# Kernel optimization log

Hardware: AMD Instinct MI355X
Metric: run time of the kernel (lower is better)

The kernel has to match this reference:

```python
import jax, jax.numpy as jnp
import numpy as np

D = 4096
L = 24
H = 8
HD = D // H
Z_TAU = 3.0
SCALE = 1.0 / float(np.sqrt(HD))


def _ln(x, w=None, b=None, eps=1e-5):
    # torch F.layer_norm over last dim; affine optional
    m = jnp.mean(x, axis=-1, keepdims=True)
    v = jnp.var(x, axis=-1, keepdims=True)
    y = (x - m) * jax.lax.rsqrt(v + eps)
    if w is not None:
        y = y * w + b
    return y


def setup_inputs() -> dict:
    key = jax.random.key(0)
    ks = jax.random.split(key, 16)
    T, N = 512, 2048
    s = 0.02  # init scale for weights
    inp = {
        'text_features': jax.random.normal(ks[0], (T, D), jnp.float32),
        'layer_features': jax.random.normal(ks[1], (L, N, D), jnp.float32),
        # DynamicSharingUnit params
        'layer_embed': jax.random.normal(ks[2], (L, D), jnp.float32) * s,
        'Wc_w': jax.random.normal(ks[3], (2 * D, D), jnp.float32) * s,
        'Wc_b': jnp.zeros((D,), jnp.float32),
        'Wz_w': jax.random.normal(ks[4], (4 * D, D), jnp.float32) * s,
        'Wz_b': jnp.full((D,), -2.0, jnp.float32),
        # SpatialGate params (delta MLP + alpha)
        'd1_w': jax.random.normal(ks[5], (D, D), jnp.float32) * s,
        'd1_b': jnp.zeros((D,), jnp.float32),
        'd2_w': jax.random.normal(ks[6], (D, D), jnp.float32) * s,
        'd2_b': jnp.zeros((D,), jnp.float32),
        'alpha': jnp.asarray(0.5, jnp.float32),
        # attention projections
        'Wq_w': jax.random.normal(ks[7], (D, D), jnp.float32) * s,
        'Wq_b': jnp.zeros((D,), jnp.float32),
        'Wk_w': jax.random.normal(ks[8], (D, D), jnp.float32) * s,
        'Wk_b': jnp.zeros((D,), jnp.float32),
        'Wo_w': jax.random.normal(ks[9], (D, D), jnp.float32) * s,
        'Wo_b': jnp.zeros((D,), jnp.float32),
        # layernorm affine params
        'qn_w': jnp.ones((D,), jnp.float32), 'qn_b': jnp.zeros((D,), jnp.float32),
        'kn_w': jnp.ones((D,), jnp.float32), 'kn_b': jnp.zeros((D,), jnp.float32),
        'vn_w': jnp.ones((D,), jnp.float32), 'vn_b': jnp.zeros((D,), jnp.float32),
        'on_w': jnp.ones((D,), jnp.float32), 'on_b': jnp.zeros((D,), jnp.float32),
    }
    return inp


def reference(text_features, layer_features, layer_embed, Wc_w, Wc_b, Wz_w, Wz_b,
              d1_w, d1_b, d2_w, d2_b, alpha,
              Wq_w, Wq_b, Wk_w, Wk_b, Wo_w, Wo_b,
              qn_w, qn_b, kn_w, kn_b, vn_w, vn_b, on_w, on_b):
    T = text_features.shape[0]
    dt = text_features.dtype

    text_global = _ln(jnp.mean(text_features, axis=0))  # [D]
    y = jnp.mean(layer_features, axis=1)                # [L, D] per-layer means

    # sequential 24-step DynamicSharingUnit recurrence
    def step(c_prev, xs):
        y_l, e_l = xs
        c_tilde = jnp.tanh(jnp.concatenate([y_l, e_l], axis=-1) @ Wc_w + Wc_b)
        z_logit = jnp.concatenate([y_l, c_prev, e_l, text_global], axis=-1) @ Wz_w + Wz_b
        z = jax.nn.sigmoid(z_logit / Z_TAU)
        c_l = c_prev + z * (c_tilde - c_prev)
        return c_l, c_l

    c0 = jnp.zeros((D,), dt)
    _, contexts = jax.lax.scan(step, c0, (y, layer_embed))  # [L, D]

    c_23 = contexts[-2]            # context after layer index 22
    pre_23 = layer_features[-2]    # [N, D]

    # SpatialGate: x + tanh(alpha) * tanh(MLP(LN(x + c)))
    h = _ln(pre_23 + c_23[None, :])
    delta = jnp.tanh(jax.nn.gelu(h @ d1_w + d1_b, approximate=False) @ d2_w + d2_b)
    refreshed = pre_23 + jnp.tanh(alpha) * delta  # [N, D]

    Q = _ln(text_features @ Wq_w + Wq_b, qn_w, qn_b)  # [T, D]
    K = _ln(refreshed @ Wk_w + Wk_b, kn_w, kn_b)      # [N, D]
    V = _ln(refreshed, vn_w, vn_b)                    # [N, D]

    q = Q.reshape(T, H, HD)
    k = K.reshape(-1, H, HD)
    v = V.reshape(-1, H, HD)
    scores = jnp.einsum('thd,nhd->htn', q, k) * SCALE  # [H, T, N]
    w = jax.nn.softmax(scores, axis=-1)
    attn = jnp.einsum('htn,nhd->thd', w, v).reshape(T, D)

    return _ln(attn @ Wo_w + Wo_b, on_w, on_b)  # [T, D]
```

## Files before the change

kernel.cpp:

```cpp
#include <hip/hip_runtime.h>
#include <hip/hip_bf16.h>

constexpr int D_  = 4096;
constexpr int L_  = 24;
constexpr int T_  = 512;
constexpr int N_  = 2048;
constexpr int H_  = 8;
constexpr int HD_ = 512;
constexpr float SCALE_ = 0.04419417382415922f;

typedef __attribute__((ext_vector_type(8))) short short8;
typedef __attribute__((ext_vector_type(4))) float f32x4;

__device__ __forceinline__ unsigned short f2b(float f){
  union{float f; unsigned u;} v; v.f=f;
  return (unsigned short)((v.u + 0x7fffu + ((v.u>>16)&1u))>>16);
}
__device__ __forceinline__ float b2f(unsigned short h){
  union{unsigned u; float f;} v; v.u=((unsigned)h)<<16; return v.f;
}

__device__ __forceinline__ void gload_lds16(const unsigned short* g, unsigned short* l){
  __builtin_amdgcn_global_load_lds((const __attribute__((address_space(1))) unsigned int*)g,
                                   (__attribute__((address_space(3))) unsigned int*)l, 16, 0, 0);
}

struct TP5 { const float* in[5]; unsigned short* out[5]; };

__global__ void prepass_all(TP5 a, const float* __restrict__ wzc_f,
                            unsigned short* __restrict__ wzcb,
                            const float* __restrict__ text,
                            unsigned short* __restrict__ txb){
  const int z = blockIdx.z, t = threadIdx.x;
  if(z < 5){
    __shared__ float tile[64][65];
    const float* in = a.in[z];
    unsigned short* out = a.out[z];
    const int k0 = blockIdx.x*64, n0 = blockIdx.y*64;
    const int tr = t>>6, tc = t&63;
#pragma unroll
    for(int i=0;i<16;++i) tile[i*4+tr][tc] = in[(size_t)(k0+i*4+tr)*D_ + n0+tc];
    __syncthreads();
#pragma unroll
    for(int i=0;i<16;++i) out[(size_t)(n0+i*4+tr)*D_ + k0+tc] = f2b(tile[tc][i*4+tr]);
  } else {
    const int bb = blockIdx.y*64 + blockIdx.x;
    const float* in; unsigned short* out; size_t base;
    if(z < 7){ in = wzc_f; out = wzcb; base = ((size_t)(z-5)*4096 + bb)*2048 + (size_t)t*8; }
    else { if(bb >= 1024) return; in = text; out = txb; base = (size_t)bb*2048 + (size_t)t*8; }
    const float4 x0 = *(const float4*)(in + base);
    const float4 x1 = *(const float4*)(in + base + 4);
    unsigned short o[8] __attribute__((aligned(16)));
    o[0]=f2b(x0.x);o[1]=f2b(x0.y);o[2]=f2b(x0.z);o[3]=f2b(x0.w);
    o[4]=f2b(x1.x);o[5]=f2b(x1.y);o[6]=f2b(x1.z);o[7]=f2b(x1.w);
    *(uint4*)(out + base) = *(const uint4*)o;
  }
}

__global__ void transpose_head_b(const unsigned short* __restrict__ in,
                                 unsigned short* __restrict__ out){
  __shared__ unsigned short tile[64][65];
  const int t = threadIdx.x;
  const int h = blockIdx.z;
  const int d0 = blockIdx.x*64, n0 = blockIdx.y*64;
  const int tr = t>>6, tc = t&63;
#pragma unroll
  for(int i=0;i<16;++i) tile[i*4+tr][tc] = in[(size_t)(n0+i*4+tr)*D_ + h*HD_ + d0+tc];
  __syncthreads();
#pragma unroll
  for(int i=0;i<16;++i) out[((size_t)h*HD_ + d0+i*4+tr)*N_ + n0+tc] = tile[tc][i*4+tr];
}

__global__ void colsum_all(const float* __restrict__ layers, const float* __restrict__ text,
                           float* __restrict__ part){
  const int d = blockIdx.x*256 + threadIdx.x;
  const int s = blockIdx.y, z = blockIdx.z;
  const float* p; int rows;
  if(z < 23){ p = layers + (size_t)z*N_*D_ + (size_t)s*(N_/8)*D_ + d; rows = N_/8; }
  else      { p = text + (size_t)s*(T_/8)*D_ + d; rows = T_/8; }
  float acc = 0.f;
  for(int r=0;r<rows;++r) acc += p[(size_t)r*D_];
  part[((size_t)z*8 + s)*D_ + d] = acc;
}

__global__ void reduce_y_gm(const float* __restrict__ part, float* __restrict__ y,
                            float* __restrict__ tg){
  __shared__ float sm[256];
  const int b = blockIdx.x, t = threadIdx.x;
  if(b < 368){
    const int i = b*256 + t, l = i>>12, j = i & (D_-1);
    float a = 0.f;
#pragma unroll
    for(int s=0;s<8;++s) a += part[((size_t)l*8 + s)*D_ + j];
    y[i] = a * (1.f/N_);
    return;
  }
  float v[16]; float sum = 0.f;
#pragma unroll
  for(int c=0;c<16;++c){
    const int j = c*256 + t;
    float a = 0.f;
#pragma unroll
    for(int s=0;s<8;++s) a += part[((size_t)184 + s)*D_ + j];
    v[c] = a * (1.f/T_); sum += v[c];
  }
  sm[t]=sum; __syncthreads();
  for(int o=128;o>0;o>>=1){ if(t<o) sm[t]+=sm[t+o]; __syncthreads(); }
  const float mean = sm[0]*(1.f/D_); __syncthreads();
  float q=0.f;
#pragma unroll
  for(int c=0;c<16;++c){ const float dd=v[c]-mean; q+=dd*dd; }
  sm[t]=q; __syncthreads();
  for(int o=128;o>0;o>>=1){ if(t<o) sm[t]+=sm[t+o]; __syncthreads(); }
  const float rstd = rsqrtf(sm[0]*(1.f/D_) + 1e-5f);
#pragma unroll
  for(int c=0;c<16;++c) tg[c*256+t] = (v[c]-mean)*rstd;
}

__global__ void smallm_all(const float* __restrict__ Wc, const float* __restrict__ Wz,
                           const float* __restrict__ y, const float* __restrict__ e,
                           const float* __restrict__ tg,
                           float* __restrict__ part0, float* __restrict__ part1){
  const int j = blockIdx.x*256 + threadIdx.x;
  const int sIdx = blockIdx.y;
  const bool w1 = (sIdx >= 16);
  const int s = w1 ? sIdx-16 : sIdx;
  const float* W = w1 ? Wz : Wc;
  const int k0 = s * 512;
  float acc[L_];
#pragma unroll
  for(int l=0;l<L_;++l) acc[l]=0.f;
  __shared__ float xs[L_][64];
  for(int kc=0; kc<512; kc+=64){
    __syncthreads();
    for(int i=threadIdx.x; i<L_*64; i+=256){
      const int l=i>>6, kk=i&63, k=k0+kc+kk;
      float xv;
      if(!w1) xv = (k<D_)? y[(size_t)l*D_+k] : e[(size_t)l*D_ + (k-D_)];
      else    xv = (k<D_)? y[(size_t)l*D_+k]
                : ((k<2*D_)? e[(size_t)l*D_ + (k-D_)] : tg[k-2*D_]);
      xs[l][kk]=xv;
    }
    __syncthreads();
    for(int kk=0;kk<64;++kk){
      const int k=k0+kc+kk;
      const int wrow = w1 ? ((k<D_)? k : k+D_) : k;
      const float wv = W[(size_t)wrow*D_ + j];
#pragma unroll
      for(int l=0;l<L_;++l) acc[l] += xs[l][kk]*wv;
    }
  }
  float* out = w1 ? part1 : part0;
  const int S = w1 ? 24 : 16;
  for(int l=0;l<L_;++l) out[((size_t)l*S + s)*D_ + j] = acc[l];
}

__global__ void reduce_ct_aall(const float* __restrict__ part0, const float* __restrict__ part1,
                               const float* __restrict__ Wcb, const float* __restrict__ Wzb,
                               float* __restrict__ ct, float* __restrict__ aall){
  int b = blockIdx.x;
  const int t = threadIdx.x;
  if(b < 368){
    const int i = b*256+t, l = i>>12, j = i & (D_-1);
    float a = 0.f;
#pragma unroll
    for(int s=0;s<16;++s) a += part0[((size_t)l*16 + s)*D_ + j];
    ct[i] = tanhf(a + Wcb[j]);
  } else {
    b -= 368;
    const int i = b*256+t, l = i>>12, j = i & (D_-1);
    float a = 0.f;
#pragma unroll
    for(int s=0;s<24;++s) a += part1[((size_t)l*24 + s)*D_ + j];
    aall[i] = a + Wzb[j];
  }
}

__device__ __forceinline__ void rec_matvec(const unsigned short* __restrict__ Wzc,
                                           const float* cs, float* red, float* __restrict__ zcur,
                                           int cg, int ks, int t){
  const int k0 = ks*128;
  float acc[8];
#pragma unroll
  for(int q=0;q<8;++q) acc[q]=0.f;
  const int rg = t>>6, oc = t&63;
  const unsigned short* Wb = Wzc + (size_t)(k0+rg*32)*D_ + cg*512 + oc*8;
#pragma unroll
  for(int rr=0;rr<4;++rr){
#pragma unroll
    for(int r=0;r<8;++r){
      const uint4 wv = *(const uint4*)(Wb + (size_t)(rr*8+r)*D_);
      const float cv = cs[rg*32+rr*8+r];
      acc[0]+=cv*b2f((unsigned short)(wv.x&0xffffu));
      acc[1]+=cv*b2f((unsigned short)(wv.x>>16));
      acc[2]+=cv*b2f((unsigned short)(wv.y&0xffffu));
      acc[3]+=cv*b2f((unsigned short)(wv.y>>16));
      acc[4]+=cv*b2f((unsigned short)(wv.z&0xffffu));
      acc[5]+=cv*b2f((unsigned short)(wv.z>>16));
      acc[6]+=cv*b2f((unsigned short)(wv.w&0xffffu));
      acc[7]+=cv*b2f((unsigned short)(wv.w>>16));
    }
  }
#pragma unroll
  for(int q=0;q<8;++q) red[rg*512 + oc*8 + q] = acc[q];
  __syncthreads();
  float s0=0.f, s1=0.f;
#pragma unroll
  for(int g=0;g<4;++g){ s0 += red[g*512 + t]; s1 += red[g*512 + t + 256]; }
  zcur[(size_t)ks*D_ + cg*512 + t]       = s0;
  zcur[(size_t)ks*D_ + cg*512 + t + 256] = s1;
}

__global__ __launch_bounds__(256,2) void rec_first(
    const unsigned short* __restrict__ Wzc, const float* __restrict__ aall0,
    const float* __restrict__ ct0, float* __restrict__ zcur, float* __restrict__ cnew){
  const int blk = blockIdx.x, cg = blk & 7, ks = blk >> 3, t = threadIdx.x;
  const int k0 = ks*128;
  __shared__ float cs[128];
  __shared__ float red[4*512];
  if(t<128){
    const float zl = aall0[k0+t];
    const float z = 1.f/(1.f+expf(-zl*(1.f/3.f)));
    const float cn = z*ct0[k0+t];
    cs[t]=cn; if(cg==0) cnew[k0+t]=cn;
  }
  __syncthreads();
  rec_matvec(Wzc, cs, red, zcur, cg, ks, t);
}

__global__ __launch_bounds__(256,2) void rec_step(
    const unsigned short* __restrict__ Wzc,
    const float* __restrict__ zprev, float* __restrict__ zcur,
    const float* __restrict__ cprev, float* __restrict__ cnew,
    const float* __restrict__ aallL, const float* __restrict__ ctL){
  const int blk = blockIdx.x, cg = blk & 7, ks = blk >> 3, t = threadIdx.x;
  const int k0 = ks*128;
  __shared__ float cs[128];
  __shared__ float red[4*512];
  {
    const int col = t & 127, hf = t >> 7;
    float s=0.f;
#pragma unroll
    for(int si=0;si<16;++si) s += zprev[(size_t)(hf*16+si)*D_ + k0 + col];
    red[hf*128+col] = s;
    __syncthreads();
    if(t<128){
      const float zl = aallL[k0+t] + red[t] + red[128+t];
      const float z = 1.f/(1.f+expf(-zl*(1.f/3.f)));
      const float cp = cprev[k0+t];
      const float cn = cp + z*(ctL[k0+t]-cp);
      cs[t]=cn;
      if(cg==0) cnew[k0+t]=cn;
    }
  }
  __syncthreads();
  rec_matvec(Wzc, cs, red, zcur, cg, ks, t);
}

__global__ void gate_final(const float* __restrict__ zp, const float* __restrict__ cin,
                           const float* __restrict__ aallL, const float* __restrict__ ctL,
                           float* __restrict__ cout){
  const int j = blockIdx.x*256 + threadIdx.x;
  float zl = aallL[j];
  for(int s=0;s<32;++s) zl += zp[(size_t)s*D_ + j];
  const float z = 1.f/(1.f + expf(-zl*(1.f/3.f)));
  const float cp = cin[j];
  cout[j] = cp + z*(ctL[j] - cp);
}

__device__ __forceinline__ void ln_body(const float* xr, const float* cvec,
                                        const float* w, const float* b,
                                        float* of, unsigned short* ob,
                                        bool addc, bool aff, bool obf, float* sm, int t){
  float v[16]; float s=0.f;
#pragma unroll
  for(int i=0;i<16;++i){
    const int d = i*256 + t;
    float val = xr[d];
    if(addc) val += cvec[d];
    v[i]=val; s+=val;
  }
  sm[t]=s; __syncthreads();
  for(int o=128;o>0;o>>=1){ if(t<o) sm[t]+=sm[t+o]; __syncthreads(); }
  const float mean = sm[0]*(1.f/D_); __syncthreads();
  float q=0.f;
#pragma unroll
  for(int i=0;i<16;++i){ const float dd=v[i]-mean; q+=dd*dd; }
  sm[t]=q; __syncthreads();
  for(int o=128;o>0;o>>=1){ if(t<o) sm[t]+=sm[t+o]; __syncthreads(); }
  const float rstd = rsqrtf(sm[0]*(1.f/D_) + 1e-5f);
#pragma unroll
  for(int i=0;i<16;++i){
    const int d = i*256+t;
    float yv=(v[i]-mean)*rstd;
    if(aff) yv = yv*w[d] + b[d];
    if(obf) ob[d] = f2b(yv);
    else    of[d] = yv;
  }
}

template<bool ADDC, bool AFF, bool OBF>
__global__ void row_ln(const float* __restrict__ x, const float* __restrict__ cvec,
                       const float* __restrict__ w, const float* __restrict__ b,
                       float* __restrict__ of, unsigned short* __restrict__ ob){
  __shared__ float sm[256];
  const int row = blockIdx.x, t = threadIdx.x;
  ln_body(x + (size_t)row*D_, cvec, w, b,
          of? of + (size_t)row*D_ : nullptr, ob? ob + (size_t)row*D_ : nullptr,
          ADDC, AFF, OBF, sm, t);
}

__global__ void ln3(const float* __restrict__ qpre, const float* __restrict__ refr,
                    const float* __restrict__ kpre,
                    const float* __restrict__ qnw, const float* __restrict__ qnb,
                    const float* __restrict__ vnw, const float* __restrict__ vnb,
                    const float* __restrict__ knw, const float* __restrict__ knb,
                    unsigned short* __restrict__ qb, unsigned short* __restrict__ vb,
                    unsigned short* __restrict__ kb){
  __shared__ float sm[256];
  const int which = blockIdx.y, row = blockIdx.x, t = threadIdx.x;
  const float *x, *w, *b; unsigned short* o;
  if(which==0){ if(row>=T_) return; x=qpre; w=qnw; b=qnb; o=qb; }
  else if(which==1){ x=refr; w=vnw; b=vnb; o=vb; }
  else { x=kpre; w=knw; b=knb; o=kb; }
  ln_body(x + (size_t)row*D_, nullptr, w, b, nullptr, o + (size_t)row*D_,
          false, true, true, sm, t);
}

__global__ void softmax_rows(unsigned short* __restrict__ wb){
  __shared__ float sm[256];
  const size_t base = (size_t)blockIdx.x * N_;
  const int t = threadIdx.x;
  float v[8];
  float mx = -3.4e38f;
#pragma unroll
  for(int i=0;i<8;++i){ v[i]=b2f(wb[base + i*256 + t]); mx=fmaxf(mx,v[i]); }
  sm[t]=mx; __syncthreads();
  for(int o=128;o>0;o>>=1){ if(t<o) sm[t]=fmaxf(sm[t],sm[t+o]); __syncthreads(); }
  mx=sm[0]; __syncthreads();
  float s=0.f;
#pragma unroll
  for(int i=0;i<8;++i){ v[i]=expf(v[i]-mx); s+=v[i]; }
  sm[t]=s; __syncthreads();
  for(int o=128;o>0;o>>=1){ if(t<o) sm[t]+=sm[t+o]; __syncthreads(); }
  const float inv = 1.f/sm[0];
#pragma unroll
  for(int i=0;i<8;++i) wb[base + i*256 + t] = f2b(v[i]*inv);
}

enum { EPI_F32_BIAS=0, EPI_BF16_GELU=1, EPI_SPATIAL=2, EPI_BF16_SCALE=3, EPI_BF16=4 };

constexpr int GBK=32;

template<int EPI, int WM>
__global__ __launch_bounds__(256,2) void gemm_bt(
  const unsigned short* __restrict__ A, const unsigned short* __restrict__ BT,
  const float* __restrict__ bias,
  float* __restrict__ Cf, unsigned short* __restrict__ Cb,
  int M, int Ncols, int K, int lda, int ldb, int ldc,
  long long aZ, long long bZ, long long cZ,
  const float* __restrict__ pre, const float* __restrict__ alphap, float scale)
{
  constexpr int BMt = WM*64;
  constexpr int NF  = WM*2;
  __shared__ unsigned short As[BMt*GBK];
  __shared__ unsigned short Bs[128*GBK];
  const int t = threadIdx.x;
  const int lane = t&63, wid = t>>6;
  const int m0 = blockIdx.x*BMt, n0 = blockIdx.y*128;
  A  += (size_t)blockIdx.z*aZ;
  BT += (size_t)blockIdx.z*bZ;
  const size_t coff = (size_t)blockIdx.z*cZ;

  const int srow = wid*16 + (lane>>2);
  const int scol = (lane&3)*8;
  const unsigned short* ag = A  + (size_t)(m0+srow)*lda + scol;
  const unsigned short* bg = BT + (size_t)(n0+srow)*ldb + scol;
  unsigned short* asl = &As[wid*512];
  unsigned short* bsl = &Bs[wid*512];

  f32x4 acc[4][NF];
#pragma unroll
  for(int i=0;i<4;++i)
#pragma unroll
    for(int j=0;j<NF;++j) acc[i][j]=(f32x4){0.f,0.f,0.f,0.f};

  const int wm = (WM==2)? (wid>>1)*64 : 0;
  const int wn = (WM==2)? (wid&1)*64 : wid*32;
  const int lrow=lane&15, lk=(lane>>4)*8;

  for(int k0=0;k0<K;k0+=GBK){
    __syncthreads();
    gload_lds16(ag + k0, asl);
    if(WM==2) gload_lds16(ag + k0 + (size_t)64*lda, asl + 2048);
    gload_lds16(bg + k0, bsl);
    gload_lds16(bg + k0 + (size_t)64*ldb, bsl + 2048);
    __syncthreads();
    short8 af[4], bfr[NF];
#pragma unroll
    for(int i=0;i<4;++i)  af[i]  = *(const short8*)&As[(wm+i*16+lrow)*GBK + lk];
#pragma unroll
    for(int j=0;j<NF;++j) bfr[j] = *(const short8*)&Bs[(wn+j*16+lrow)*GBK + lk];
#pragma unroll
    for(int i=0;i<4;++i)
#pragma unroll
      for(int j=0;j<NF;++j)
        acc[i][j] = __builtin_amdgcn_mfma_f32_16x16x32_bf16(af[i], bfr[j], acc[i][j], 0,0,0);
  }

  float ta=0.f;
  if(EPI==EPI_SPATIAL) ta = tanhf(alphap[0]);
#pragma unroll
  for(int i=0;i<4;++i)
#pragma unroll
    for(int j=0;j<NF;++j){
      const int col = n0 + wn + j*16 + lrow;
      const int rb  = m0 + wm + i*16 + (lane>>4)*4;
#pragma unroll
      for(int r=0;r<4;++r){
        const int row = rb + r;
        const float v = acc[i][j][r];
        const size_t idx = coff + (size_t)row*ldc + col;
        if(EPI==EPI_F32_BIAS){ Cf[idx] = v + bias[col]; }
        else if(EPI==EPI_BF16_GELU){
          const float x=v+bias[col];
          Cb[idx]=f2b(0.5f*x*(1.f+erff(x*0.70710678118f)));
        }
        else if(EPI==EPI_SPATIAL){
          const float x=tanhf(v+bias[col]);
          const float o= pre[(size_t)row*ldc+col] + ta*x;
          Cf[idx]=o; Cb[idx]=f2b(o);
        }
        else if(EPI==EPI_BF16_SCALE){ Cb[idx]=f2b(v*scale); }
        else { Cb[idx]=f2b(v); }
      }
    }
}

constexpr int P_SLOT_A = 128*64;
constexpr int P_SLOT_B = 256*64;
constexpr int P_SLOT_E = P_SLOT_A + P_SLOT_B;

#define MF16(a,b,c) __builtin_amdgcn_mfma_f32_16x16x32_bf16(a,b,c,0,0,0)

template<int EPI, bool SWZ>
__global__ __launch_bounds__(512,2) void gemm8p(
    const unsigned short* __restrict__ A, const unsigned short* __restrict__ BT,
    const float* __restrict__ bias,
    float* __restrict__ Cf, unsigned short* __restrict__ Cb,
    int K, int lda, int ldb, int ldc,
    long long aZ, long long bZ, long long cZ,
    const float* __restrict__ pre, const float* __restrict__ alphap, float scale)
{
  __shared__ unsigned short lds[3*P_SLOT_E];
  const int tid = threadIdx.x;
  const int lane = tid & 63, wid = tid >> 6;
  int mi, ni, zi;
  if(SWZ){
    const int b = blockIdx.x;
    const int swz = (b & 7)*32 + (b >> 3);
    mi = swz >> 4; ni = swz & 15; zi = 0;
  } else { mi = blockIdx.x; ni = blockIdx.y; zi = blockIdx.z; }
  const int m0 = mi*128, n0 = ni*256;
  A  += (size_t)zi*aZ;
  BT += (size_t)zi*bZ;
  const size_t coff = (size_t)zi*cZ;

  const int wm = (wid >> 2)*64, wn = (wid & 3)*64;
  const int lr = lane & 15, lhi = lane >> 4;

  auto stage = [&](int slot, int kt){
    const int k0 = kt*64;
    unsigned short* sA = lds + slot*P_SLOT_E;
    unsigned short* sB = sA + P_SLOT_A;
#pragma unroll
    for(int q=0;q<2;++q){
      const int o = q*8192 + tid*16;
      const int r = o >> 7;
      const int cb = (o & 127) ^ ((r & 7) << 4);
      gload_lds16(A + (size_t)(m0+r)*lda + k0 + (cb>>1), sA + q*4096 + wid*512);
    }
#pragma unroll
    for(int q=0;q<4;++q){
      const int o = q*8192 + tid*16;
      const int r = o >> 7;
      const int cb = (o & 127) ^ ((r & 7) << 4);
      gload_lds16(BT + (size_t)(n0+r)*ldb + k0 + (cb>>1), sB + q*4096 + wid*512);
    }
  };

  auto ldA = [&](const unsigned short* sA, int i, int ks)->short8{
    const int ra = wm + i*16 + lr;
    const int cb = (ks*64 + lhi*16) ^ ((ra & 7) << 4);
    return *(const short8*)((const char*)sA + ra*128 + cb);
  };
  auto ldB = [&](const unsigned short* sB, int j, int ks)->short8{
    const int rb = wn + j*16 + lr;
    const int cb = (ks*64 + lhi*16) ^ ((rb & 7) << 4);
    return *(const short8*)((const char*)sB + rb*128 + cb);
  };

  f32x4 acc[4][4];
#pragma unroll
  for(int i=0;i<4;++i)
#pragma unroll
    for(int j=0;j<4;++j) acc[i][j]=(f32x4){0.f,0.f,0.f,0.f};

  auto tile_compute = [&](const unsigned short* sA, const unsigned short* sB){
#pragma unroll
    for(int ks=0; ks<2; ++ks){
      short8 a0=ldA(sA,0,ks), a1=ldA(sA,1,ks), a2=ldA(sA,2,ks), a3=ldA(sA,3,ks);
      short8 b0=ldB(sB,0,ks), b1=ldB(sB,1,ks);
      __builtin_amdgcn_s_setprio(1);
      acc[0][0]=MF16(a0,b0,acc[0][0]); acc[1][0]=MF16(a1,b0,acc[1][0]);
      acc[2][0]=MF16(a2,b0,acc[2][0]); acc[3][0]=MF16(a3,b0,acc[3][0]);
      acc[0][1]=MF16(a0,b1,acc[0][1]); acc[1][1]=MF16(a1,b1,acc[1][1]);
      acc[2][1]=MF16(a2,b1,acc[2][1]); acc[3][1]=MF16(a3,b1,acc[3][1]);
      __builtin_amdgcn_s_setprio(0);
      __builtin_amdgcn_s_barrier();
      short8 b2=ldB(sB,2,ks), b3=ldB(sB,3,ks);
      __builtin_amdgcn_s_setprio(1);
      acc[0][2]=MF16(a0,b2,acc[0][2]); acc[1][2]=MF16(a1,b2,acc[1][2]);
      acc[2][2]=MF16(a2,b2,acc[2][2]); acc[3][2]=MF16(a3,b2,acc[3][2]);
      acc[0][3]=MF16(a0,b3,acc[0][3]); acc[1][3]=MF16(a1,b3,acc[1][3]);
      acc[2][3]=MF16(a2,b3,acc[2][3]); acc[3][3]=MF16(a3,b3,acc[3][3]);
      __builtin_amdgcn_s_setprio(0);
      if(ks==0) __builtin_amdgcn_s_barrier();
    }
  };

  const int nt = K >> 6;
  stage(0, 0);
  stage(1, 1);
  int cur = 0;
  for(int t=0; t<nt-1; ++t){
    asm volatile("s_waitcnt vmcnt(6)" ::: "memory");
    __builtin_amdgcn_s_barrier();
    int s2 = cur+2; if(s2>=3) s2-=3;
    if(t+2 < nt) stage(s2, t+2);
    const unsigned short* sA = lds + cur*P_SLOT_E;
    tile_compute(sA, sA + P_SLOT_A);
    ++cur; if(cur==3) cur=0;
  }
  asm volatile("s_waitcnt vmcnt(0)" ::: "memory");
  __builtin_amdgcn_s_barrier();
  {
    const unsigned short* sA = lds + cur*P_SLOT_E;
    tile_compute(sA, sA + P_SLOT_A);
  }

  float ta=0.f;
  if(EPI==EPI_SPATIAL) ta = tanhf(alphap[0]);
#pragma unroll
  for(int i=0;i<4;++i)
#pragma unroll
    for(int j=0;j<4;++j){
      const int col = n0 + wn + j*16 + lr;
      const int rb  = m0 + wm + i*16 + lhi*4;
#pragma unroll
      for(int r=0;r<4;++r){
        const int row = rb + r;
        const float v = acc[i][j][r];
        const size_t idx = coff + (size_t)row*ldc + col;
        if(EPI==EPI_F32_BIAS){ Cf[idx] = v + bias[col]; }
        else if(EPI==EPI_BF16_GELU){
          const float x = v + bias[col];
          Cb[idx] = f2b(0.5f*x*(1.f+erff(x*0.70710678118f)));
        }
        else if(EPI==EPI_SPATIAL){
          const float x = tanhf(v + bias[col]);
          const float o = pre[idx] + ta*x;
          Cf[idx]=o; Cb[idx]=f2b(o);
        }
        else if(EPI==EPI_BF16_SCALE){ Cb[idx]=f2b(v*scale); }
      }
    }
}

constexpr size_t OFF_TG   = 0;
constexpr size_t OFF_C    = OFF_TG + (size_t)D_*4;
constexpr size_t OFF_Y    = OFF_C  + (size_t)D_*4;
constexpr size_t OFF_CT   = OFF_Y  + (size_t)L_*D_*4;
constexpr size_t OFF_AA   = OFF_CT + (size_t)L_*D_*4;
constexpr size_t OFF_ZP0  = OFF_AA + (size_t)L_*D_*4;
constexpr size_t OFF_ZP1  = OFF_ZP0 + (size_t)32*D_*4;
constexpr size_t OFF_PART = OFF_ZP1 + (size_t)32*D_*4;
constexpr size_t OFF_QPRE = OFF_PART + (size_t)24*L_*D_*4;
constexpr size_t OFF_REFR = OFF_QPRE + (size_t)T_*D_*4;
constexpr size_t OFF_HB   = OFF_REFR + (size_t)N_*D_*4;
constexpr size_t OFF_G1   = OFF_HB + (size_t)N_*D_*2;
constexpr size_t OFF_KPRE = OFF_HB;
constexpr size_t OFF_QB   = OFF_G1 + (size_t)N_*D_*2;
constexpr size_t OFF_KB   = OFF_QB + (size_t)T_*D_*2;
constexpr size_t OFF_VB   = OFF_KB + (size_t)N_*D_*2;
constexpr size_t OFF_VT   = OFF_VB + (size_t)N_*D_*2;
constexpr size_t OFF_WB   = OFF_VT + (size_t)H_*HD_*N_*2;
constexpr size_t OFF_ATTN = OFF_WB + (size_t)H_*T_*N_*2;
constexpr size_t OFF_W1T  = OFF_ATTN + (size_t)T_*D_*2;
constexpr size_t OFF_W2T  = OFF_W1T + (size_t)D_*D_*2;
constexpr size_t OFF_WKT  = OFF_W2T + (size_t)D_*D_*2;
constexpr size_t OFF_WQT  = OFF_WKT + (size_t)D_*D_*2;
constexpr size_t OFF_WOT  = OFF_WQT + (size_t)D_*D_*2;
constexpr size_t OFF_WZCB = OFF_WOT + (size_t)D_*D_*2;
constexpr size_t OFF_TXB  = OFF_WZCB + (size_t)D_*D_*2;
constexpr size_t OFF_REFB = OFF_TXB + (size_t)T_*D_*2;
constexpr size_t OFF_CA   = OFF_REFB + (size_t)N_*D_*2;
constexpr size_t OFF_CB   = OFF_CA + (size_t)D_*4;

extern "C" void kernel_launch(void* const* d_in, const int* in_sizes, int n_in,
                              void* d_out, int out_size, void* d_ws, size_t ws_size,
                              hipStream_t stream){
  (void)in_sizes; (void)n_in; (void)out_size; (void)ws_size;
  const float* text  = (const float*)d_in[0];
  const float* layers= (const float*)d_in[1];
  const float* le    = (const float*)d_in[2];
  const float* Wc    = (const float*)d_in[3];
  const float* Wcb   = (const float*)d_in[4];
  const float* Wz    = (const float*)d_in[5];
  const float* Wzb   = (const float*)d_in[6];
  const float* d1w   = (const float*)d_in[7];
  const float* d1b   = (const float*)d_in[8];
  const float* d2w   = (const float*)d_in[9];
  const float* d2b   = (const float*)d_in[10];
  const float* alpha = (const float*)d_in[11];
  const float* Wqw=(const float*)d_in[12]; const float* Wqb=(const float*)d_in[13];
  const float* Wkw=(const float*)d_in[14]; const float* Wkb=(const float*)d_in[15];
  const float* Wow=(const float*)d_in[16]; const float* Wob=(const float*)d_in[17];
  const float* qnw=(const float*)d_in[18]; const float* qnb=(const float*)d_in[19];
  const float* knw=(const float*)d_in[20]; const float* knb=(const float*)d_in[21];
  const float* vnw=(const float*)d_in[22]; const float* vnb=(const float*)d_in[23];
  const float* onw=(const float*)d_in[24]; const float* onb=(const float*)d_in[25];
  float* out = (float*)d_out;

  char* w = (char*)d_ws;
  float* tg    = (float*)(w + OFF_TG);
  float* cvec  = (float*)(w + OFF_C);
  float* y     = (float*)(w + OFF_Y);
  float* ct    = (float*)(w + OFF_CT);
  float* aall  = (float*)(w + OFF_AA);
  float* zp0   = (float*)(w + OFF_ZP0);
  float* zp1   = (float*)(w + OFF_ZP1);
  float* part  = (float*)(w + OFF_PART);
  float* part1 = part + (size_t)384*D_;
  float* qpre  = (float*)(w + OFF_QPRE);
  float* opre  = qpre;
  float* refr  = (float*)(w + OFF_REFR);
  float* kpre  = (float*)(w + OFF_KPRE);
  float* cA    = (float*)(w + OFF_CA);
  float* cB    = (float*)(w + OFF_CB);
  unsigned short* hb    = (unsigned short*)(w + OFF_HB);
  unsigned short* g1    = (unsigned short*)(w + OFF_G1);
  unsigned short* qb    = (unsigned short*)(w + OFF_QB);
  unsigned short* kb    = (unsigned short*)(w + OFF_KB);
  unsigned short* vb    = (unsigned short*)(w + OFF_VB);
  unsigned short* vt    = (unsigned short*)(w + OFF_VT);
  unsigned short* wb    = (unsigned short*)(w + OFF_WB);
  unsigned short* attnb = (unsigned short*)(w + OFF_ATTN);
  unsigned short* d1t   = (unsigned short*)(w + OFF_W1T);
  unsigned short* d2t   = (unsigned short*)(w + OFF_W2T);
  unsigned short* wkt   = (unsigned short*)(w + OFF_WKT);
  unsigned short* wqt   = (unsigned short*)(w + OFF_WQT);
  unsigned short* wot   = (unsigned short*)(w + OFF_WOT);
  unsigned short* wzcb  = (unsigned short*)(w + OFF_WZCB);
  unsigned short* txb   = (unsigned short*)(w + OFF_TXB);
  unsigned short* refb  = (unsigned short*)(w + OFF_REFB);

  const dim3 b256(256);
  const float* pre23 = layers + (size_t)(L_-2)*N_*D_;

  TP5 tp; tp.in[0]=d1w; tp.in[1]=d2w; tp.in[2]=Wkw; tp.in[3]=Wqw; tp.in[4]=Wow;
  tp.out[0]=d1t; tp.out[1]=d2t; tp.out[2]=wkt; tp.out[3]=wqt; tp.out[4]=wot;
  prepass_all<<<dim3(64,64,8),b256,0,stream>>>(tp, Wz + (size_t)D_*D_, wzcb, text, txb);

  colsum_all<<<dim3(16,8,24),b256,0,stream>>>(layers, text, part);
  reduce_y_gm<<<dim3(369),b256,0,stream>>>(part, y, tg);
  smallm_all<<<dim3(16,40),b256,0,stream>>>(Wc, Wz, y, le, tg, part, part1);
  reduce_ct_aall<<<dim3(736),b256,0,stream>>>(part, part1, Wcb, Wzb, ct, aall);

  rec_first<<<dim3(256),b256,0,stream>>>(wzcb, aall, ct, zp0, cA);
  for(int i=1;i<L_-2;++i){
    float* zprev = (i&1)? zp0 : zp1;
    float* zcur  = (i&1)? zp1 : zp0;
    float* cprev = (i&1)? cA  : cB;
    float* cnew  = (i&1)? cB  : cA;
    rec_step<<<dim3(256),b256,0,stream>>>(wzcb, zprev, zcur, cprev, cnew,
        aall + (size_t)i*D_, ct + (size_t)i*D_);
  }
  gate_final<<<dim3(16),b256,0,stream>>>(zp1, cB,
      aall + (size_t)(L_-2)*D_, ct + (size_t)(L_-2)*D_, cvec);

  row_ln<true,false,true><<<dim3(N_),b256,0,stream>>>(pre23, cvec, nullptr,nullptr, nullptr, hb);
  gemm8p<EPI_BF16_GELU,true><<<dim3(256),dim3(512),0,stream>>>(
      hb, d1t, d1b, nullptr, g1, D_, D_, D_, D_, 0,0,0, nullptr,nullptr,0.f);
  gemm8p<EPI_SPATIAL,true><<<dim3(256),dim3(512),0,stream>>>(
      g1, d2t, d2b, refr, refb, D_, D_, D_, D_, 0,0,0, pre23, alpha, 0.f);

  gemm8p<EPI_F32_BIAS,false><<<dim3(4,16,1),dim3(512),0,stream>>>(
      txb, wqt, Wqb, qpre, nullptr, D_, D_, D_, D_, 0,0,0, nullptr,nullptr,0.f);
  gemm8p<EPI_F32_BIAS,true><<<dim3(256),dim3(512),0,stream>>>(
      refb, wkt, Wkb, kpre, nullptr, D_, D_, D_, D_, 0,0,0, nullptr,nullptr,0.f);

  ln3<<<dim3(N_,3),b256,0,stream>>>(qpre, refr, kpre,
      qnw,qnb, vnw,vnb, knw,knb, qb, vb, kb);
  transpose_head_b<<<dim3(8,32,8),b256,0,stream>>>(vb, vt);

  gemm8p<EPI_BF16_SCALE,false><<<dim3(4,8,8),dim3(512),0,stream>>>(
      qb, kb, nullptr, nullptr, wb, HD_, D_, D_, N_,
      (long long)HD_, (long long)HD_, (long long)T_*N_, nullptr,nullptr, SCALE_);
  softmax_rows<<<dim3(H_*T_),b256,0,stream>>>(wb);
  gemm_bt<EPI_BF16,1><<<dim3(8,4,8),b256,0,stream>>>(
      wb, vt, nullptr, nullptr, attnb, T_, HD_, N_, N_, N_, D_,
      (long long)T_*N_, (long long)HD_*N_, (long long)HD_, nullptr,nullptr,0.f);

  gemm8p<EPI_F32_BIAS,false><<<dim3(4,16,1),dim3(512),0,stream>>>(
      attnb, wot, Wob, opre, nullptr, D_, D_, D_, D_, 0,0,0, nullptr,nullptr,0.f);
  row_ln<false,true,false><<<dim3(T_),b256,0,stream>>>(opre, nullptr, onw, onb, out, nullptr);
}
```

Before: 1.247 ms.

## Split-K the Q and output projection GEMMs with partial-sum reduction fused into LayerNorm

The T=512 Q and output projection GEMMs previously launched only 64 workgroups, which leaves most compute units idle. They now split K into four chunks of 1024, launching 256 workgroups, each writing raw fp32 partials to separate slices. The four partials plus bias are summed inside the following LayerNorm kernels (ln3 and a new row_ln_out). This adds extra fp32 partial-buffer traffic and a larger scratch region in exchange for better CU occupancy. Unused epilogue branches of gemm_bt were also removed.

```diff
diff --git a/kernel.cpp b/kernel.cpp
--- a/kernel.cpp
+++ b/kernel.cpp
@@ -268,18 +268,12 @@
   cout[j] = cp + z*(ctL[j] - cp);
 }
 
-__device__ __forceinline__ void ln_body(const float* xr, const float* cvec,
-                                        const float* w, const float* b,
+__device__ __forceinline__ void ln_vals(float* v, const float* w, const float* b,
                                         float* of, unsigned short* ob,
-                                        bool addc, bool aff, bool obf, float* sm, int t){
-  float v[16]; float s=0.f;
-#pragma unroll
-  for(int i=0;i<16;++i){
-    const int d = i*256 + t;
-    float val = xr[d];
-    if(addc) val += cvec[d];
-    v[i]=val; s+=val;
-  }
+                                        bool aff, bool obf, float* sm, int t){
+  float s=0.f;
+#pragma unroll
+  for(int i=0;i<16;++i) s += v[i];
   sm[t]=s; __syncthreads();
   for(int o=128;o>0;o>>=1){ if(t<o) sm[t]+=sm[t+o]; __syncthreads(); }
   const float mean = sm[0]*(1.f/D_); __syncthreads();
@@ -305,13 +299,21 @@
                        float* __restrict__ of, unsigned short* __restrict__ ob){
   __shared__ float sm[256];
   const int row = blockIdx.x, t = threadIdx.x;
-  ln_body(x + (size_t)row*D_, cvec, w, b,
-          of? of + (size_t)row*D_ : nullptr, ob? ob + (size_t)row*D_ : nullptr,
-          ADDC, AFF, OBF, sm, t);
+  const float* xr = x + (size_t)row*D_;
+  float v[16];
+#pragma unroll
+  for(int i=0;i<16;++i){
+    const int d = i*256 + t;
+    float val = xr[d];
+    if(ADDC) val += cvec[d];
+    v[i]=val;
+  }
+  ln_vals(v, w, b, of? of + (size_t)row*D_ : nullptr,
+          ob? ob + (size_t)row*D_ : nullptr, AFF, OBF, sm, t);
 }
 
 __global__ void ln3(const float* __restrict__ qpre, const float* __restrict__ refr,
-                    const float* __restrict__ kpre,
+                    const float* __restrict__ kpre, const float* __restrict__ qpb,
                     const float* __restrict__ qnw, const float* __restrict__ qnb,
                     const float* __restrict__ vnw, const float* __restrict__ vnb,
                     const float* __restrict__ knw, const float* __restrict__ knb,
@@ -319,12 +321,43 @@
                     unsigned short* __restrict__ kb){
   __shared__ float sm[256];
   const int which = blockIdx.y, row = blockIdx.x, t = threadIdx.x;
-  const float *x, *w, *b; unsigned short* o;
-  if(which==0){ if(row>=T_) return; x=qpre; w=qnw; b=qnb; o=qb; }
-  else if(which==1){ x=refr; w=vnw; b=vnb; o=vb; }
-  else { x=kpre; w=knw; b=knb; o=kb; }
-  ln_body(x + (size_t)row*D_, nullptr, w, b, nullptr, o + (size_t)row*D_,
-          false, true, true, sm, t);
+  float v[16];
+  if(which==0){
+    if(row>=T_) return;
+    const float* x0 = qpre + (size_t)row*D_;
+#pragma unroll
+    for(int i=0;i<16;++i){
+      const int d = i*256+t;
+      v[i] = x0[d] + x0[(size_t)T_*D_ + d] + x0[(size_t)2*T_*D_ + d]
+           + x0[(size_t)3*T_*D_ + d] + qpb[d];
+    }
+    ln_vals(v, qnw, qnb, nullptr, qb + (size_t)row*D_, true, true, sm, t);
+  } else {
+    const float* x = (which==1)? refr : kpre;
+    const float* w = (which==1)? vnw : knw;
+    const float* b = (which==1)? vnb : knb;
+    unsigned short* o = (which==1)? vb : kb;
+    const float* xr = x + (size_t)row*D_;
+#pragma unroll
+    for(int i=0;i<16;++i) v[i] = xr[i*256+t];
+    ln_vals(v, w, b, nullptr, o + (size_t)row*D_, true, true, sm, t);
+  }
+}
+
+__global__ void row_ln_out(const float* __restrict__ opre, const float* __restrict__ opb,
+                           const float* __restrict__ w, const float* __restrict__ b,
+                           float* __restrict__ out){
+  __shared__ float sm[256];
+  const int row = blockIdx.x, t = threadIdx.x;
+  const float* x0 = opre + (size_t)row*D_;
+  float v[16];
+#pragma unroll
+  for(int i=0;i<16;++i){
+    const int d = i*256+t;
+    v[i] = x0[d] + x0[(size_t)T_*D_ + d] + x0[(size_t)2*T_*D_ + d]
+         + x0[(size_t)3*T_*D_ + d] + opb[d];
+  }
+  ln_vals(v, w, b, out + (size_t)row*D_, nullptr, true, false, sm, t);
 }
 
 __global__ void softmax_rows(unsigned short* __restrict__ wb){
@@ -348,7 +381,7 @@
   for(int i=0;i<8;++i) wb[base + i*256 + t] = f2b(v[i]*inv);
 }
 
-enum { EPI_F32_BIAS=0, EPI_BF16_GELU=1, EPI_SPATIAL=2, EPI_BF16_SCALE=3, EPI_BF16=4 };
+enum { EPI_F32_BIAS=0, EPI_BF16_GELU=1, EPI_SPATIAL=2, EPI_BF16_SCALE=3, EPI_BF16=4, EPI_F32_RAW=5 };
 
 constexpr int GBK=32;
 
@@ -408,8 +441,6 @@
         acc[i][j] = __builtin_amdgcn_mfma_f32_16x16x32_bf16(af[i], bfr[j], acc[i][j], 0,0,0);
   }
 
-  float ta=0.f;
-  if(EPI==EPI_SPATIAL) ta = tanhf(alphap[0]);
 #pragma unroll
   for(int i=0;i<4;++i)
 #pragma unroll
@@ -422,16 +453,6 @@
         const float v = acc[i][j][r];
         const size_t idx = coff + (size_t)row*ldc + col;
         if(EPI==EPI_F32_BIAS){ Cf[idx] = v + bias[col]; }
-        else if(EPI==EPI_BF16_GELU){
-          const float x=v+bias[col];
-          Cb[idx]=f2b(0.5f*x*(1.f+erff(x*0.70710678118f)));
-        }
-        else if(EPI==EPI_SPATIAL){
-          const float x=tanhf(v+bias[col]);
-          const float o= pre[(size_t)row*ldc+col] + ta*x;
-          Cf[idx]=o; Cb[idx]=f2b(o);
-        }
-        else if(EPI==EPI_BF16_SCALE){ Cb[idx]=f2b(v*scale); }
         else { Cb[idx]=f2b(v); }
       }
     }
@@ -563,6 +584,7 @@
         const float v = acc[i][j][r];
         const size_t idx = coff + (size_t)row*ldc + col;
         if(EPI==EPI_F32_BIAS){ Cf[idx] = v + bias[col]; }
+        else if(EPI==EPI_F32_RAW){ Cf[idx] = v; }
         else if(EPI==EPI_BF16_GELU){
           const float x = v + bias[col];
           Cb[idx] = f2b(0.5f*x*(1.f+erff(x*0.70710678118f)));
@@ -586,7 +608,7 @@
 constexpr size_t OFF_ZP1  = OFF_ZP0 + (size_t)32*D_*4;
 constexpr size_t OFF_PART = OFF_ZP1 + (size_t)32*D_*4;
 constexpr size_t OFF_QPRE = OFF_PART + (size_t)24*L_*D_*4;
-constexpr size_t OFF_REFR = OFF_QPRE + (size_t)T_*D_*4;
+constexpr size_t OFF_REFR = OFF_QPRE + (size_t)4*T_*D_*4;
 constexpr size_t OFF_HB   = OFF_REFR + (size_t)N_*D_*4;
 constexpr size_t OFF_G1   = OFF_HB + (size_t)N_*D_*2;
 constexpr size_t OFF_KPRE = OFF_HB;
@@ -695,12 +717,13 @@
   gemm8p<EPI_SPATIAL,true><<<dim3(256),dim3(512),0,stream>>>(
       g1, d2t, d2b, refr, refb, D_, D_, D_, D_, 0,0,0, pre23, alpha, 0.f);
 
-  gemm8p<EPI_F32_BIAS,false><<<dim3(4,16,1),dim3(512),0,stream>>>(
-      txb, wqt, Wqb, qpre, nullptr, D_, D_, D_, D_, 0,0,0, nullptr,nullptr,0.f);
+  gemm8p<EPI_F32_RAW,false><<<dim3(4,16,4),dim3(512),0,stream>>>(
+      txb, wqt, nullptr, qpre, nullptr, 1024, D_, D_, D_,
+      1024, 1024, (long long)T_*D_, nullptr,nullptr,0.f);
   gemm8p<EPI_F32_BIAS,true><<<dim3(256),dim3(512),0,stream>>>(
       refb, wkt, Wkb, kpre, nullptr, D_, D_, D_, D_, 0,0,0, nullptr,nullptr,0.f);
 
-  ln3<<<dim3(N_,3),b256,0,stream>>>(qpre, refr, kpre,
+  ln3<<<dim3(N_,3),b256,0,stream>>>(qpre, refr, kpre, Wqb,
       qnw,qnb, vnw,vnb, knw,knb, qb, vb, kb);
   transpose_head_b<<<dim3(8,32,8),b256,0,stream>>>(vb, vt);
 
@@ -712,7 +735,8 @@
       wb, vt, nullptr, nullptr, attnb, T_, HD_, N_, N_, N_, D_,
       (long long)T_*N_, (long long)HD_*N_, (long long)HD_, nullptr,nullptr,0.f);
 
-  gemm8p<EPI_F32_BIAS,false><<<dim3(4,16,1),dim3(512),0,stream>>>(
-      attnb, wot, Wob, opre, nullptr, D_, D_, D_, D_, 0,0,0, nullptr,nullptr,0.f);
-  row_ln<false,true,false><<<dim3(T_),b256,0,stream>>>(opre, nullptr, onw, onb, out, nullptr);
-}
+  gemm8p<EPI_F32_RAW,false><<<dim3(4,16,4),dim3(512),0,stream>>>(
+      attnb, wot, nullptr, opre, nullptr, 1024, D_, D_, D_,
+      1024, 1024, (long long)T_*D_, nullptr,nullptr,0.f);
+  row_ln_out<<<dim3(T_),b256,0,stream>>>(opre, Wob, onw, onb, out);
+}
```

Result: faster. 1.173 ms (-5.9%).
